# Performance work log

Measured on AMD Instinct MI355X. Metric: run time of the kernel, lower is better.

Reference implementation:

```python
import math
import jax, jax.numpy as jnp
import numpy as np

K = 2                 # top-k gate
CAP_FACTOR = 1.0      # capacity_factor
EPS = 1e-9


def setup_inputs() -> dict:
    key = jax.random.key(0)
    ks = jax.random.split(key, 6)
    B, S, D, H, E = 4, 2048, 1024, 4096, 8
    x = jax.random.normal(ks[0], (B, S, D), jnp.float32)
    wg = jax.random.normal(ks[1], (D, E), jnp.float32) * 0.02
    w1 = jax.random.normal(ks[2], (E, D, H), jnp.float32) * 0.02
    b1 = jnp.zeros((E, H), jnp.float32)
    w2 = jax.random.normal(ks[3], (E, H, D), jnp.float32) * 0.02
    b2 = jnp.zeros((E, D), jnp.float32)
    return {"x": x, "wg": wg, "w1": w1, "b1": b1, "w2": w2, "b2": b2}


def reference(x, wg, w1, b1, w2, b2):
    B, S, D = x.shape
    E = wg.shape[1]
    xt = x.reshape(-1, D)                      # [N, D] tokens
    N = xt.shape[0]
    cap = int(math.ceil(CAP_FACTOR * K * N / E))

    # fp32 gate: softmax scores, top-k selection, normalized gates
    logits = xt.astype(jnp.float32) @ wg.astype(jnp.float32)    # [N, E]
    scores = jax.nn.softmax(logits, axis=-1)
    gvals, gidx = jax.lax.top_k(scores, K)                      # [N, K]
    gvals = gvals / jnp.clip(gvals.sum(-1, keepdims=True), EPS)

    # GShard-style capacity locations: k-th choice offset by earlier choices' counts
    offset = jnp.zeros((E,), jnp.int32)
    pos_l, keep_l = [], []
    for kk in range(K):
        m = jax.nn.one_hot(gidx[:, kk], E, dtype=jnp.int32)     # [N, E]
        loc = jnp.cumsum(m, axis=0) - 1 + offset[None, :]
        offset = offset + m.sum(axis=0)
        pos = jnp.take_along_axis(loc, gidx[:, kk:kk + 1], axis=1)[:, 0]
        keep = pos < cap
        pos_l.append(jnp.where(keep, pos, 0))
        keep_l.append(keep)
    pos = jnp.stack(pos_l, axis=1)             # [N, K]
    keep = jnp.stack(keep_l, axis=1)           # [N, K] bool
    gvals = gvals * keep                       # drop overflowed tokens

    e_flat = gidx.reshape(-1)                  # [N*K]
    p_flat = pos.reshape(-1)
    kmask = keep.reshape(-1).astype(x.dtype)
    x_rep = jnp.repeat(xt, K, axis=0)          # [N*K, D], token-major matches reshape

    # dispatch (scatter to expert slots); postscore=True -> no gate weight here
    disp = jnp.zeros((E, cap, D), x.dtype).at[e_flat, p_flat].add(x_rep * kmask[:, None])

    # grouped expert FFN with exact GELU
    h = jax.nn.gelu(jnp.einsum('ecd,edh->ech', disp, w1) + b1[:, None, :], approximate=False)
    y = jnp.einsum('ech,ehd->ecd', h, w2) + b2[:, None, :]      # [E, cap, D]

    # combine (gather + gate-weighted sum over k)
    yk = y[e_flat, p_flat]                                      # [N*K, D]
    w = gvals.reshape(-1).astype(x.dtype)
    out = (yk * w[:, None]).reshape(N, K, D).sum(axis=1)
    return out.reshape(B, S, D)
```

## Files before the change

kernel.cpp:

```cpp
#include <hip/hip_runtime.h>
#include <hip/hip_bf16.h>
#include <math.h>

#define N_TOK 8192
#define DIM   1024
#define HID   4096
#define NEXP  8
#define CAP   2048

typedef short bf16x8 __attribute__((ext_vector_type(8)));
typedef float f32x4  __attribute__((ext_vector_type(4)));

__device__ __forceinline__ unsigned short f2bf(float f) {
    union { float f; unsigned u; } v; v.f = f;
    unsigned r = v.u;
    unsigned lsb = (r >> 16) & 1u;
    r += 0x7fffu + lsb;
    return (unsigned short)(r >> 16);
}

__device__ __forceinline__ float gelu_f(float v) {
    float az = fabsf(v);
    float z  = az * 0.70710678118654752f;
    float t  = __builtin_amdgcn_rcpf(fmaf(0.3275911f, z, 1.0f));
    float p  = fmaf(fmaf(fmaf(fmaf(1.061405429f, t, -1.453152027f),
                               t, 1.421413741f), t, -0.284496736f), t, 0.254829592f) * t;
    float ez = __expf(-z * z);
    float q5 = 0.5f * p * ez;
    float phi = (v >= 0.f) ? (1.f - q5) : q5;
    return v * phi;
}

__global__ __launch_bounds__(256) void init_kernel(int* __restrict__ slot_token) {
    int gid = blockIdx.x * 256 + threadIdx.x;
    slot_token[gid] = -1;
}

__global__ __launch_bounds__(256) void transpose_convert_kernel(
        const float* __restrict__ in, unsigned short* __restrict__ outp,
        int R, int C) {
    int e  = blockIdx.z;
    int c0 = blockIdx.x * 64, r0 = blockIdx.y * 64;
    __shared__ float tile[64][65];
    const float* ip = in + (size_t)e * R * C;
    unsigned short* op = outp + (size_t)e * R * C;
    int t = threadIdx.x;
    int rr = t >> 4, cc = (t & 15) * 4;
    #pragma unroll
    for (int p = 0; p < 4; ++p) {
        f32x4 v = *(const f32x4*)(ip + (size_t)(r0 + p * 16 + rr) * C + c0 + cc);
        tile[p * 16 + rr][cc + 0] = v[0];
        tile[p * 16 + rr][cc + 1] = v[1];
        tile[p * 16 + rr][cc + 2] = v[2];
        tile[p * 16 + rr][cc + 3] = v[3];
    }
    __syncthreads();
    int ct = t >> 4, rq = (t & 15) * 4;
    #pragma unroll
    for (int p = 0; p < 4; ++p) {
        int c = p * 16 + ct;
        ushort4 o;
        o.x = f2bf(tile[rq + 0][c]);
        o.y = f2bf(tile[rq + 1][c]);
        o.z = f2bf(tile[rq + 2][c]);
        o.w = f2bf(tile[rq + 3][c]);
        *(ushort4*)(op + (size_t)(c0 + c) * R + r0 + rq) = o;
    }
}

__global__ __launch_bounds__(256) void gate_kernel(
        const float* __restrict__ x, const float* __restrict__ wg,
        int* __restrict__ tok_e, float* __restrict__ tok_g) {
    int wave = threadIdx.x >> 6, lane = threadIdx.x & 63;
    int n = blockIdx.x * 4 + wave;
    const float* xr = x + (size_t)n * DIM;
    float acc[8];
    #pragma unroll
    for (int e = 0; e < 8; ++e) acc[e] = 0.f;
    for (int j = 0; j < DIM / 64; ++j) {
        int d = lane + 64 * j;
        float xv = xr[d];
        const f32x4* wr = (const f32x4*)(wg + (size_t)d * 8);
        f32x4 w0 = wr[0], w1 = wr[1];
        acc[0] += xv * w0[0]; acc[1] += xv * w0[1];
        acc[2] += xv * w0[2]; acc[3] += xv * w0[3];
        acc[4] += xv * w1[0]; acc[5] += xv * w1[1];
        acc[6] += xv * w1[2]; acc[7] += xv * w1[3];
    }
    #pragma unroll
    for (int off = 32; off > 0; off >>= 1) {
        #pragma unroll
        for (int e = 0; e < 8; ++e) acc[e] += __shfl_down(acc[e], off);
    }
    if (lane == 0) {
        float mx = acc[0];
        #pragma unroll
        for (int e = 1; e < 8; ++e) mx = fmaxf(mx, acc[e]);
        float p[8], s = 0.f;
        #pragma unroll
        for (int e = 0; e < 8; ++e) { p[e] = expf(acc[e] - mx); s += p[e]; }
        int i0 = 0;
        #pragma unroll
        for (int e = 1; e < 8; ++e) if (acc[e] > acc[i0]) i0 = e;
        int i1 = (i0 == 0) ? 1 : 0;
        #pragma unroll
        for (int e = 0; e < 8; ++e) if (e != i0 && acc[e] > acc[i1]) i1 = e;
        float g0 = p[i0] / s, g1 = p[i1] / s;
        float gs = fmaxf(g0 + g1, 1e-9f);
        tok_e[n * 2 + 0] = i0;  tok_e[n * 2 + 1] = i1;
        tok_g[n * 2 + 0] = g0 / gs;  tok_g[n * 2 + 1] = g1 / gs;
    }
}

__global__ __launch_bounds__(512) void route_kernel(
        const int* __restrict__ tok_e,
        int* __restrict__ slot_token, int* __restrict__ tok_slot) {
    __shared__ int te[N_TOK];
    int w = threadIdx.x >> 6;
    int lane = threadIdx.x & 63;
    unsigned long long below = (lane == 63) ? 0x7fffffffffffffffull
                                            : ((1ull << lane) - 1ull);
    int cnt = 0;
    for (int kk = 0; kk < 2; ++kk) {
        __syncthreads();
        for (int i = threadIdx.x; i < N_TOK; i += 512) te[i] = tok_e[i * 2 + kk];
        __syncthreads();
        #pragma unroll 4
        for (int base = 0; base < N_TOK; base += 64) {
            int n = base + lane;
            bool mine = (te[n] == w);
            unsigned long long m = __ballot(mine);
            if (mine) {
                int pos = cnt + __popcll(m & below);
                bool ok = pos < CAP;
                tok_slot[n * 2 + kk] = ok ? (w * CAP + pos) : -1;
                if (ok) slot_token[w * CAP + pos] = n;
            }
            cnt += __popcll(m);
        }
    }
}

__global__ __launch_bounds__(256) void dispatch_kernel(
        const float* __restrict__ x, const int* __restrict__ slot_token,
        unsigned short* __restrict__ disp) {
    int s = blockIdx.x;
    int tok = slot_token[s];
    int t = threadIdx.x;
    unsigned short* dp = disp + (size_t)s * DIM + t * 4;
    uint2 o;
    if (tok < 0) { o.x = 0u; o.y = 0u; }
    else {
        const f32x4 v = *(const f32x4*)(x + (size_t)tok * DIM + t * 4);
        o.x = (unsigned)f2bf(v[0]) | ((unsigned)f2bf(v[1]) << 16);
        o.y = (unsigned)f2bf(v[2]) | ((unsigned)f2bf(v[3]) << 16);
    }
    *(uint2*)dp = o;
}

template<int KD>
__device__ __forceinline__ void mainloop256(
        const unsigned short* __restrict__ Ag, const unsigned short* __restrict__ Bg,
        unsigned short* lds, f32x4 (&acc)[8][4]) {
    const int t = threadIdx.x;
    const int w = t >> 6, l = t & 63;
    const int wm = w >> 2, wn = w & 3;

    const int slot0 = w * 64 + l;
    const int slot1 = 512 + w * 64 + l;
    const int r0 = (slot0 >> 6) * 16 + (slot0 & 15), c0 = (slot0 >> 4) & 3;
    const int r1 = (slot1 >> 6) * 16 + (slot1 & 15), c1 = (slot1 >> 4) & 3;
    const size_t ofs0 = (size_t)r0 * KD + c0 * 8;
    const size_t ofs1 = (size_t)r1 * KD + c1 * 8;
    const int dst0 = (w * 64) * 8;
    const int dst1 = (512 + w * 64) * 8;

    auto stage = [&](const unsigned short* G, int ldsbase, int kh, int kt) {
        __builtin_amdgcn_global_load_lds(
            (const __attribute__((address_space(1))) void*)(G + ofs0 + kt + kh * 32),
            (__attribute__((address_space(3))) void*)(lds + ldsbase + kh * 8192 + dst0), 16, 0, 0);
        __builtin_amdgcn_global_load_lds(
            (const __attribute__((address_space(1))) void*)(G + ofs1 + kt + kh * 32),
            (__attribute__((address_space(3))) void*)(lds + ldsbase + kh * 8192 + dst1), 16, 0, 0);
    };
    auto ldA = [&](int abase, int ks, int m) {
        return *(const bf16x8*)(lds + abase + ks * 8192 + (wm * 8 + m) * 512 + l * 8);
    };
    auto ldB = [&](int bbase, int ks, int n) {
        return *(const bf16x8*)(lds + bbase + ks * 8192 + (wn * 4 + n) * 512 + l * 8);
    };

#define MFMA_PAIR(nlo)                                                                     \
    __builtin_amdgcn_s_setprio(1);                                                         \
    _Pragma("unroll")                                                                      \
    for (int m = 0; m < 8; ++m) {                                                          \
        acc[m][nlo]     = __builtin_amdgcn_mfma_f32_16x16x32_bf16(af[m], bf[nlo],     acc[m][nlo],     0, 0, 0); \
        acc[m][nlo + 1] = __builtin_amdgcn_mfma_f32_16x16x32_bf16(af[m], bf[nlo + 1], acc[m][nlo + 1], 0, 0, 0); \
    }                                                                                      \
    __builtin_amdgcn_s_setprio(0);

    constexpr int NT = KD / 64;
    bf16x8 af[8], bf[4];

    stage(Ag, 0, 0, 0);  stage(Bg, 16384, 0, 0);
    stage(Ag, 0, 1, 0);  stage(Bg, 16384, 1, 0);

    int cur = 0;
#pragma unroll 1
    for (int T = 0; T < NT; ++T, cur ^= 1) {
        const int abase = cur * 32768, bbase = abase + 16384;
        const int nA = (cur ^ 1) * 32768, nB = nA + 16384;
        const int ktn = (T + 1) * 64;
        const bool pf = (T + 1 < NT);

        asm volatile("s_waitcnt vmcnt(4)\n\ts_barrier" ::: "memory");
        #pragma unroll
        for (int m = 0; m < 8; ++m) af[m] = ldA(abase, 0, m);
        bf[0] = ldB(bbase, 0, 0);  bf[1] = ldB(bbase, 0, 1);
        if (pf) stage(Ag, nA, 0, ktn);
        MFMA_PAIR(0)
        bf[2] = ldB(bbase, 0, 2);  bf[3] = ldB(bbase, 0, 3);
        if (pf) stage(Bg, nB, 0, ktn);
        MFMA_PAIR(2)
        if (pf) { asm volatile("s_waitcnt vmcnt(4)\n\ts_barrier" ::: "memory"); }
        else    { asm volatile("s_waitcnt vmcnt(0)\n\ts_barrier" ::: "memory"); }
        #pragma unroll
        for (int m = 0; m < 8; ++m) af[m] = ldA(abase, 1, m);
        bf[0] = ldB(bbase, 1, 0);  bf[1] = ldB(bbase, 1, 1);
        if (pf) stage(Ag, nA, 1, ktn);
        MFMA_PAIR(0)
        bf[2] = ldB(bbase, 1, 2);  bf[3] = ldB(bbase, 1, 3);
        if (pf) stage(Bg, nB, 1, ktn);
        MFMA_PAIR(2)
    }
#undef MFMA_PAIR
}

__global__ __launch_bounds__(512, 2) void gemm1_kernel(
        const unsigned short* __restrict__ disp, const unsigned short* __restrict__ w1t,
        const float* __restrict__ b1, unsigned short* __restrict__ h) {
    extern __shared__ unsigned short lds[];
    constexpr int TOT = (CAP / 256) * (HID / 256) * NEXP;
    constexpr int TPE = (CAP / 256) * (HID / 256);
    constexpr int TN  = HID / 256;
    const int bid = (blockIdx.x & 7) * (TOT >> 3) + (blockIdx.x >> 3);
    const int e = bid / TPE, tt = bid % TPE, tm = tt / TN, tn = tt % TN;

    const unsigned short* A = disp + ((size_t)e * CAP + tm * 256) * DIM;
    const unsigned short* B = w1t  + ((size_t)e * HID + tn * 256) * DIM;
    f32x4 acc[8][4];
    #pragma unroll
    for (int m = 0; m < 8; ++m)
        #pragma unroll
        for (int n = 0; n < 4; ++n) acc[m][n] = (f32x4){0.f, 0.f, 0.f, 0.f};

    mainloop256<DIM>(A, B, lds, acc);

    const int l = threadIdx.x & 63, w = threadIdx.x >> 6;
    const int l16 = l & 15, kh4 = l >> 4;
    const int wm = w >> 2, wn = w & 3;
    const float* b1e = b1 + (size_t)e * HID + tn * 256;
    float bias[4];
    #pragma unroll
    for (int n = 0; n < 4; ++n) bias[n] = b1e[wn * 64 + n * 16 + l16];
    unsigned short* H = h + ((size_t)e * CAP + tm * 256) * HID + tn * 256;
    #pragma unroll
    for (int m = 0; m < 8; ++m)
        #pragma unroll
        for (int n = 0; n < 4; ++n)
            #pragma unroll
            for (int r = 0; r < 4; ++r) {
                int row = wm * 128 + m * 16 + kh4 * 4 + r;
                int col = wn * 64 + n * 16 + l16;
                H[(size_t)row * HID + col] = f2bf(gelu_f(acc[m][n][r] + bias[n]));
            }
}

__global__ __launch_bounds__(512, 2) void gemm2_kernel(
        const unsigned short* __restrict__ h, const unsigned short* __restrict__ w2t,
        const float* __restrict__ b2, float* __restrict__ y) {
    extern __shared__ unsigned short lds[];
    constexpr int TOT = (CAP / 256) * (DIM / 256) * NEXP;
    constexpr int TPE = (CAP / 256) * (DIM / 256);
    constexpr int TN  = DIM / 256;
    const int bid = (blockIdx.x & 7) * (TOT >> 3) + (blockIdx.x >> 3);
    const int e = bid / TPE, tt = bid % TPE, tm = tt / TN, tn = tt % TN;

    const unsigned short* A = h   + ((size_t)e * CAP + tm * 256) * HID;
    const unsigned short* B = w2t + ((size_t)e * DIM + tn * 256) * HID;
    f32x4 acc[8][4];
    #pragma unroll
    for (int m = 0; m < 8; ++m)
        #pragma unroll
        for (int n = 0; n < 4; ++n) acc[m][n] = (f32x4){0.f, 0.f, 0.f, 0.f};

    mainloop256<HID>(A, B, lds, acc);

    const int l = threadIdx.x & 63, w = threadIdx.x >> 6;
    const int l16 = l & 15, kh4 = l >> 4;
    const int wm = w >> 2, wn = w & 3;
    const float* b2e = b2 + (size_t)e * DIM + tn * 256;
    float bias[4];
    #pragma unroll
    for (int n = 0; n < 4; ++n) bias[n] = b2e[wn * 64 + n * 16 + l16];
    float* Y = y + ((size_t)e * CAP + tm * 256) * DIM + tn * 256;
    #pragma unroll
    for (int m = 0; m < 8; ++m)
        #pragma unroll
        for (int n = 0; n < 4; ++n)
            #pragma unroll
            for (int r = 0; r < 4; ++r) {
                int row = wm * 128 + m * 16 + kh4 * 4 + r;
                int col = wn * 64 + n * 16 + l16;
                Y[(size_t)row * DIM + col] = acc[m][n][r] + bias[n];
            }
}

__global__ __launch_bounds__(256) void combine_kernel(
        const float* __restrict__ y, const int* __restrict__ tok_slot,
        const float* __restrict__ tok_g, float* __restrict__ out) {
    int n = blockIdx.x, t = threadIdx.x;
    int s0 = tok_slot[n * 2], s1 = tok_slot[n * 2 + 1];
    float g0 = tok_g[n * 2], g1 = tok_g[n * 2 + 1];
    f32x4 r = {0.f, 0.f, 0.f, 0.f};
    if (s0 >= 0) {
        f32x4 v = *(const f32x4*)(y + (size_t)s0 * DIM + t * 4);
        r[0] = g0 * v[0]; r[1] = g0 * v[1]; r[2] = g0 * v[2]; r[3] = g0 * v[3];
    }
    if (s1 >= 0) {
        f32x4 v = *(const f32x4*)(y + (size_t)s1 * DIM + t * 4);
        r[0] += g1 * v[0]; r[1] += g1 * v[1]; r[2] += g1 * v[2]; r[3] += g1 * v[3];
    }
    *(f32x4*)(out + (size_t)n * DIM + t * 4) = r;
}

extern "C" void kernel_launch(void* const* d_in, const int* in_sizes, int n_in,
                              void* d_out, int out_size, void* d_ws, size_t ws_size,
                              hipStream_t stream) {
    (void)in_sizes; (void)n_in; (void)out_size; (void)ws_size;
    const float* x  = (const float*)d_in[0];
    const float* wg = (const float*)d_in[1];
    const float* w1 = (const float*)d_in[2];
    const float* b1 = (const float*)d_in[3];
    const float* w2 = (const float*)d_in[4];
    const float* b2 = (const float*)d_in[5];
    float* out = (float*)d_out;

    char* ws = (char*)d_ws;
    size_t off = 0;
    unsigned short* w1t  = (unsigned short*)(ws + off); off += (size_t)NEXP * HID * DIM * 2;
    unsigned short* w2t  = (unsigned short*)(ws + off); off += (size_t)NEXP * DIM * HID * 2;
    unsigned short* disp = (unsigned short*)(ws + off); off += (size_t)NEXP * CAP * DIM * 2;
    unsigned short* hbuf = (unsigned short*)(ws + off); off += (size_t)NEXP * CAP * HID * 2;
    int*   slot_token = (int*)  (ws + off); off += (size_t)NEXP * CAP * 4;
    int*   tok_e      = (int*)  (ws + off); off += (size_t)N_TOK * 2 * 4;
    float* tok_g      = (float*)(ws + off); off += (size_t)N_TOK * 2 * 4;
    int*   tok_slot   = (int*)  (ws + off); off += (size_t)N_TOK * 2 * 4;
    float* ybuf = (float*)w1t;

    hipFuncSetAttribute((const void*)gemm1_kernel,
                        hipFuncAttributeMaxDynamicSharedMemorySize, 131072);
    hipFuncSetAttribute((const void*)gemm2_kernel,
                        hipFuncAttributeMaxDynamicSharedMemorySize, 131072);

    hipLaunchKernelGGL(init_kernel, dim3(NEXP * CAP / 256), dim3(256), 0, stream,
                       slot_token);
    hipLaunchKernelGGL(transpose_convert_kernel, dim3(HID / 64, DIM / 64, NEXP), dim3(256), 0, stream,
                       w1, w1t, DIM, HID);
    hipLaunchKernelGGL(transpose_convert_kernel, dim3(DIM / 64, HID / 64, NEXP), dim3(256), 0, stream,
                       w2, w2t, HID, DIM);
    hipLaunchKernelGGL(gate_kernel, dim3(N_TOK / 4), dim3(256), 0, stream, x, wg, tok_e, tok_g);
    hipLaunchKernelGGL(route_kernel, dim3(1), dim3(512), 0, stream,
                       tok_e, slot_token, tok_slot);
    hipLaunchKernelGGL(dispatch_kernel, dim3(NEXP * CAP), dim3(256), 0, stream,
                       x, slot_token, disp);
    hipLaunchKernelGGL(gemm1_kernel, dim3((CAP / 256) * (HID / 256) * NEXP), dim3(512), 131072, stream,
                       disp, w1t, b1, hbuf);
    hipLaunchKernelGGL(gemm2_kernel, dim3((CAP / 256) * (DIM / 256) * NEXP), dim3(512), 131072, stream,
                       hbuf, w2t, b2, ybuf);
    hipLaunchKernelGGL(combine_kernel, dim3(N_TOK), dim3(256), 0, stream,
                       ybuf, tok_slot, tok_g, out);
}
```

Measured before the change: 709.9 us.

## Deepen GEMM LDS pipeline to prefetch two k-tiles ahead with finer barriers

```diff
diff --git a/kernel.cpp b/kernel.cpp
--- a/kernel.cpp
+++ b/kernel.cpp
@@ -190,8 +190,8 @@
         return *(const bf16x8*)(lds + bbase + ks * 8192 + (wn * 4 + n) * 512 + l * 8);
     };
 
-#define MFMA_PAIR(nlo)                                                                     \
-    __builtin_amdgcn_s_setprio(1);                                                         \
+#define MFMA16(nlo)                                                                        \
+    __builtin_amdgcn_s_setprio(1);                                                        \
     _Pragma("unroll")                                                                      \
     for (int m = 0; m < 8; ++m) {                                                          \
         acc[m][nlo]     = __builtin_amdgcn_mfma_f32_16x16x32_bf16(af[m], bf[nlo],     acc[m][nlo],     0, 0, 0); \
@@ -199,41 +199,64 @@
     }                                                                                      \
     __builtin_amdgcn_s_setprio(0);
 
+#define OPEN_SYNC                                                                          \
+    __builtin_amdgcn_sched_barrier(0);                                                     \
+    __builtin_amdgcn_s_barrier();                                                          \
+    asm volatile("s_waitcnt lgkmcnt(0)" ::: "memory");                                     \
+    __builtin_amdgcn_sched_barrier(0);
+
     constexpr int NT = KD / 64;
     bf16x8 af[8], bf[4];
 
-    stage(Ag, 0, 0, 0);  stage(Bg, 16384, 0, 0);
-    stage(Ag, 0, 1, 0);  stage(Bg, 16384, 1, 0);
-
-    int cur = 0;
+    stage(Ag, 0, 0, 0);       stage(Bg, 16384, 0, 0);
+    stage(Ag, 0, 1, 0);       stage(Bg, 16384, 1, 0);
+    if (NT > 1) {
+        stage(Ag, 32768, 0, 64);  stage(Bg, 49152, 0, 64);
+        stage(Ag, 32768, 1, 64);
+        asm volatile("s_waitcnt vmcnt(6)" ::: "memory");
+    } else {
+        asm volatile("s_waitcnt vmcnt(0)" ::: "memory");
+    }
+    __builtin_amdgcn_s_barrier();
+
 #pragma unroll 1
-    for (int T = 0; T < NT; ++T, cur ^= 1) {
+    for (int T = 0; T < NT; ++T) {
+        const int cur = T & 1;
         const int abase = cur * 32768, bbase = abase + 16384;
         const int nA = (cur ^ 1) * 32768, nB = nA + 16384;
-        const int ktn = (T + 1) * 64;
-        const bool pf = (T + 1 < NT);
-
-        asm volatile("s_waitcnt vmcnt(4)\n\ts_barrier" ::: "memory");
+
         #pragma unroll
         for (int m = 0; m < 8; ++m) af[m] = ldA(abase, 0, m);
         bf[0] = ldB(bbase, 0, 0);  bf[1] = ldB(bbase, 0, 1);
-        if (pf) stage(Ag, nA, 0, ktn);
-        MFMA_PAIR(0)
+        if (T + 1 < NT) stage(Bg, nB, 1, (T + 1) * 64);
+        OPEN_SYNC
+        MFMA16(0)
+        __builtin_amdgcn_s_barrier();
+
         bf[2] = ldB(bbase, 0, 2);  bf[3] = ldB(bbase, 0, 3);
-        if (pf) stage(Bg, nB, 0, ktn);
-        MFMA_PAIR(2)
-        if (pf) { asm volatile("s_waitcnt vmcnt(4)\n\ts_barrier" ::: "memory"); }
-        else    { asm volatile("s_waitcnt vmcnt(0)\n\ts_barrier" ::: "memory"); }
+        if (T + 2 < NT) stage(Ag, abase, 0, (T + 2) * 64);
+        OPEN_SYNC
+        MFMA16(2)
+        __builtin_amdgcn_s_barrier();
+
         #pragma unroll
         for (int m = 0; m < 8; ++m) af[m] = ldA(abase, 1, m);
         bf[0] = ldB(bbase, 1, 0);  bf[1] = ldB(bbase, 1, 1);
-        if (pf) stage(Ag, nA, 1, ktn);
-        MFMA_PAIR(0)
+        if (T + 2 < NT) stage(Bg, bbase, 0, (T + 2) * 64);
+        OPEN_SYNC
+        MFMA16(0)
+        __builtin_amdgcn_s_barrier();
+
         bf[2] = ldB(bbase, 1, 2);  bf[3] = ldB(bbase, 1, 3);
-        if (pf) stage(Bg, nB, 1, ktn);
-        MFMA_PAIR(2)
-    }
-#undef MFMA_PAIR
+        if (T + 2 < NT) stage(Ag, abase, 1, (T + 2) * 64);
+        OPEN_SYNC
+        MFMA16(2)
+        if (T < NT - 2)       { asm volatile("s_waitcnt vmcnt(6)" ::: "memory"); }
+        else if (T == NT - 2) { asm volatile("s_waitcnt vmcnt(0)" ::: "memory"); }
+        if (T < NT - 1) __builtin_amdgcn_s_barrier();
+    }
+#undef MFMA16
+#undef OPEN_SYNC
 }
 
 __global__ __launch_bounds__(512, 2) void gemm1_kernel(
```

Result: no change. 716.2 us (+0.9%).
